# Kernel tuning notes

Measured on AMD Instinct MI355X. Metric: run time of the kernel, lower is better.

## Reference

```python
import jax, jax.numpy as jnp
import numpy as np

N_NODES = 8192
N_EDGES = 81920
N_EDGE2 = 1310720
D_EMB = 128
D_GAT = 64
H = 128
N_CLASSES = 2


def setup_inputs() -> dict:
    key = jax.random.key(0)
    ks = jax.random.split(key, 18)
    s = 0.05
    return {
        "x": jax.random.normal(ks[0], (N_NODES, D_EMB), jnp.float32),
        "embed": jax.random.normal(ks[1], (N_NODES, D_EMB), jnp.float32),
        "noise": jax.random.uniform(ks[2], (N_EDGES,), jnp.float32, 1e-6, 1.0 - 1e-6),
        "tmp": jnp.ones((), jnp.float32),
        "gat_W": jax.random.normal(ks[3], (2 * D_EMB, D_GAT), jnp.float32) * s,
        "att_src": jax.random.normal(ks[4], (D_GAT,), jnp.float32) * s,
        "att_dst": jax.random.normal(ks[5], (D_GAT,), jnp.float32) * s,
        "gat_bias": jax.random.normal(ks[6], (D_GAT,), jnp.float32) * s,
        "lin_W": jax.random.normal(ks[7], (D_GAT, 1), jnp.float32) * s,
        "lin_b": jax.random.normal(ks[8], (1,), jnp.float32) * s,
        "W1": jax.random.normal(ks[9], (D_EMB, H), jnp.float32) * s,
        "W2": jax.random.normal(ks[10], (H, H), jnp.float32) * s,
        "W3": jax.random.normal(ks[11], (H, H), jnp.float32) * s,
        "Wc": jax.random.normal(ks[12], (H, N_CLASSES), jnp.float32) * s,
        "edge_index": jax.random.randint(ks[13], (2, N_EDGES), 0, N_NODES, jnp.int32),
        "new_edge_index": jax.random.randint(ks[14], (2, N_EDGE2), 0, N_EDGES, jnp.int32),
        "label": 1,
    }


def reference(x, embed, noise, tmp, gat_W, att_src, att_dst, gat_bias, lin_W, lin_b,
              W1, W2, W3, Wc, edge_index, new_edge_index, label):
    N, E = x.shape[0], edge_index.shape[1]
    row, col = edge_index[0], edge_index[1]

    # h = cat(embed[row], embed[col])  -> [E, 2D]
    h = jnp.concatenate([embed[row], embed[col]], axis=-1)

    # --- GATConv(2D, 64) over the edge-adjacency graph (PyG single-head, self-loops) ---
    hp = h @ gat_W                              # [E, D_GAT]
    a_s = hp @ att_src                          # [E]
    a_d = hp @ att_dst                          # [E]
    loop = jnp.arange(E, dtype=new_edge_index.dtype)
    src = jnp.concatenate([new_edge_index[0], loop])
    dst = jnp.concatenate([new_edge_index[1], loop])
    alpha = jax.nn.leaky_relu(a_s[src] + a_d[dst], negative_slope=0.2)
    amax = jax.ops.segment_max(alpha, dst, num_segments=E)
    ealpha = jnp.exp(alpha - amax[dst])
    denom = jax.ops.segment_sum(ealpha, dst, num_segments=E)
    attn = ealpha / denom[dst]                  # softmax per destination edge-node
    gat_out = jax.ops.segment_sum(attn[:, None] * hp[src], dst, num_segments=E) + gat_bias

    # Linear(64, 1)
    log_alpha = (gat_out @ lin_W + lin_b).reshape(-1)   # [E]

    # concrete_sample (training=True, sample_bias=0.0)
    gate = jax.nn.sigmoid((jnp.log(noise) - jnp.log1p(-noise) + log_alpha) / tmp)

    # dense adjacency (ones, coalesce-sum) and dense gated mask
    adj = jnp.zeros((N, N), jnp.float32).at[row, col].add(1.0)
    sym_mask = jnp.zeros((N, N), jnp.float32).at[row, col].add(gate)
    sym_mask = (sym_mask + sym_mask.T) * 0.5
    masked_adj = adj * sym_mask
    edge_mask = masked_adj[row, col]

    # --- stub downstream model: 3-layer edge-weighted GCN + mean pool + classifier ---
    # explain-mode edge masking: messages weighted by sigmoid(edge_mask)
    w = jax.nn.sigmoid(edge_mask)
    deg = jax.ops.segment_sum(w, col, num_segments=N) + 1.0   # [N]

    def gcn(xh, W):
        msg = jax.ops.segment_sum(w[:, None] * xh[row], col, num_segments=N)
        return jax.nn.relu(((xh + msg) / deg[:, None]) @ W)

    h1 = gcn(x, W1)
    h2 = gcn(h1, W2)
    h3 = gcn(h2, W3)
    g = h3.mean(axis=0)                         # global mean pool (single graph)
    logits = g @ Wc
    return jax.nn.softmax(logits, axis=-1)
```

## Files before the change

kernel.cpp:

```cpp
#include <hip/hip_runtime.h>
#include <hip/hip_fp16.h>
#include <math.h>

typedef unsigned long long u64;
typedef __attribute__((ext_vector_type(2))) float fv2;

#define NN 8192
#define EE 81920
#define E2C 1310720
#define HSZ (1 << 18)
#define HMASK (HSZ - 1)
#define NBIN 320
#define BCAP 4800
#define SBITS 17

__device__ __forceinline__ float wsum(float v) {
#pragma unroll
  for (int m = 32; m > 0; m >>= 1) v += __shfl_xor(v, m, 64);
  return v;
}
__device__ __forceinline__ float lrelu(float x) { return x > 0.f ? x : 0.2f * x; }
__device__ __forceinline__ unsigned packh2(float a, float b) {
  __half2 h = __floats2half2_rn(a, b);
  return *reinterpret_cast<unsigned*>(&h);
}
__device__ __forceinline__ void atomic_pk_add_f16(unsigned* addr, unsigned data) {
  asm volatile("global_atomic_pk_add_f16 %0, %1, off" :: "v"(addr), "v"(data) : "memory");
}
__device__ __forceinline__ int hfind(const int* __restrict__ keys, int key) {
  unsigned i = ((unsigned)key * 2654435761u) >> 14 & HMASK;
  while (true) {
    int k = keys[i];
    if (k == key) return (int)i;
    if (k == -1) return -1;
    i = (i + 1) & HMASK;
  }
}
__device__ __forceinline__ float2 bf2f(unsigned u) {
  return make_float2(__uint_as_float(u << 16), __uint_as_float(u & 0xffff0000u));
}
__device__ __forceinline__ unsigned f2bf(float a, float b) {
  unsigned ua = __float_as_uint(a);
  ua = (ua + 0x7fffu + ((ua >> 16) & 1u)) >> 16;
  unsigned ub = __float_as_uint(b);
  ub = ((ub + 0x7fffu + ((ub >> 16) & 1u)) >> 16) << 16;
  return (ua & 0xffffu) | ub;
}
__device__ __forceinline__ unsigned f2bf1(float a) {
  unsigned ua = __float_as_uint(a);
  return (ua + 0x7fffu + ((ua >> 16) & 1u)) >> 16;
}
__device__ __forceinline__ float bf1f(unsigned u) { return __uint_as_float(u << 16); }
__device__ __forceinline__ unsigned short f2fp8x2(float a, float b) {
  return (unsigned short)(__builtin_amdgcn_cvt_pk_fp8_f32(a, b, 0, false) & 0xffff);
}
__device__ __forceinline__ float2 fp8x2f(unsigned short v) {
  fv2 f = __builtin_amdgcn_cvt_pk_f32_fp8((int)(unsigned)v, false);
  return make_float2(f[0], f[1]);
}
__device__ __forceinline__ float rdlane(float v, int k) {
  return __uint_as_float(__builtin_amdgcn_readlane(__float_as_uint(v), k));
}

__global__ __launch_bounds__(256) void kA(const float* __restrict__ x,
                                          const float* __restrict__ embed,
                                          const float* __restrict__ gw,
                                          const float* __restrict__ att_s,
                                          const float* __restrict__ att_d,
                                          const float* __restrict__ lin_W,
                                          const float* __restrict__ gat_b,
                                          const float* __restrict__ lin_b,
                                          float4* __restrict__ pN, float4* __restrict__ qN,
                                          unsigned short* __restrict__ xbu,
                                          int* __restrict__ hKeys, unsigned* __restrict__ hPair,
                                          int* __restrict__ colCnt, float* __restrict__ gvec,
                                          unsigned* __restrict__ done, unsigned* __restrict__ gCur,
                                          float* __restrict__ gbS) {
  __shared__ float sm[768];
  int t = threadIdx.x, bid = blockIdx.x;
  int lane = t & 63, wv = t >> 6;
  for (int i = bid * 256 + t; i < HSZ; i += 512 * 256) { hKeys[i] = -1; hPair[i] = 0u; }
  for (int i = bid * 256 + t; i < NN; i += 512 * 256) colCnt[i] = 0;
  if (bid == 0) {
    for (int i = t; i < 2048; i += 256) gvec[i] = 0.f;
    if (t == 0) *done = 0u;
    for (int i = t; i < NBIN; i += 256) gCur[i] = 0u;
    if (wv == 0) {
      float gb = wsum(gat_b[lane] * lin_W[lane]);
      if (lane == 0) *gbS = gb + lin_b[0];
    }
  }
  {
    int n = bid * 16 + (t >> 4);
    int dp = (t & 15) * 8;
    const float4* x4 = (const float4*)(x + n * 128 + dp);
    float4 a = x4[0], b = x4[1];
    unsigned p0 = f2fp8x2(a.x, a.y), p1 = f2fp8x2(a.z, a.w);
    unsigned p2 = f2fp8x2(b.x, b.y), p3 = f2fp8x2(b.z, b.w);
    ((uint2*)xbu)[n * 16 + (t & 15)] = make_uint2(p0 | (p1 << 16), p2 | (p3 << 16));
  }
  {
    float sa = 0.f, sd = 0.f, sz = 0.f;
#pragma unroll 8
    for (int k = 0; k < 64; k++) {
      float w = gw[t * 64 + k];
      sa += w * att_s[k]; sd += w * att_d[k]; sz += w * lin_W[k];
    }
    sm[t] = sa; sm[256 + t] = sd; sm[512 + t] = sz;
  }
  __syncthreads();
#pragma unroll
  for (int j = 0; j < 4; j++) {
    int n = bid * 16 + wv * 4 + j;
    float e0 = embed[n * 128 + lane], e1 = embed[n * 128 + 64 + lane];
    float pA = wsum(e0 * sm[lane] + e1 * sm[64 + lane]);
    float qA = wsum(e0 * sm[128 + lane] + e1 * sm[192 + lane]);
    float pD = wsum(e0 * sm[256 + lane] + e1 * sm[320 + lane]);
    float qD = wsum(e0 * sm[384 + lane] + e1 * sm[448 + lane]);
    float pZ = wsum(e0 * sm[512 + lane] + e1 * sm[576 + lane]);
    float qZ = wsum(e0 * sm[640 + lane] + e1 * sm[704 + lane]);
    if (lane == 0) pN[n] = make_float4(pA, pD, pZ, 0.f);
    if (lane == 1) qN[n] = make_float4(qA, qD, qZ, 0.f);
  }
}

__global__ __launch_bounds__(256) void kC(const int* __restrict__ row, const int* __restrict__ col,
                                          const float4* __restrict__ pN, const float4* __restrict__ qN,
                                          float2* __restrict__ asz, float* __restrict__ ad,
                                          int* __restrict__ colCnt,
                                          const int* __restrict__ src2, const int* __restrict__ dst2,
                                          unsigned* __restrict__ gCur, unsigned* __restrict__ bucket) {
  __shared__ unsigned hist[NBIN], base[NBIN], lcur[NBIN];
  int t = threadIdx.x;
  for (int i = t; i < NBIN; i += 256) { hist[i] = 0u; lcur[i] = 0u; }
  int blockBase = blockIdx.x * 4096;
  {
    int e = blockIdx.x * 256 + t;
    int r = row[e], c = col[e];
    float4 p = pN[r];
    float4 q = qN[c];
    asz[e] = make_float2(p.x + q.x, p.z + q.z);
    ad[e] = p.y + q.y;
    atomicAdd(&colCnt[c], 1);
  }
  __syncthreads();
  int4 dv[4];
#pragma unroll
  for (int j = 0; j < 4; j++) {
    dv[j] = *(const int4*)&dst2[blockBase + j * 1024 + t * 4];
    atomicAdd(&hist[dv[j].x >> 8], 1u);
    atomicAdd(&hist[dv[j].y >> 8], 1u);
    atomicAdd(&hist[dv[j].z >> 8], 1u);
    atomicAdd(&hist[dv[j].w >> 8], 1u);
  }
  __syncthreads();
  for (int i = t; i < NBIN; i += 256)
    if (hist[i]) base[i] = atomicAdd(&gCur[i], hist[i]);
  __syncthreads();
#pragma unroll
  for (int j = 0; j < 4; j++) {
    int4 sv = *(const int4*)&src2[blockBase + j * 1024 + t * 4];
    int ss[4] = {sv.x, sv.y, sv.z, sv.w};
    int dd[4] = {dv[j].x, dv[j].y, dv[j].z, dv[j].w};
#pragma unroll
    for (int k = 0; k < 4; k++) {
      int s = ss[k], d = dd[k];
      int b = d >> 8;
      unsigned r = atomicAdd(&lcur[b], 1u);
      unsigned pos = base[b] + r;
      if (pos < BCAP) bucket[(size_t)b * BCAP + pos] = ((unsigned)(d & 255) << SBITS) | (unsigned)s;
    }
  }
}

__global__ __launch_bounds__(256) void kD(const int* __restrict__ row, const int* __restrict__ col,
                                          const float2* __restrict__ asz, const float* __restrict__ ad,
                                          const unsigned* __restrict__ bucket, const unsigned* __restrict__ gCur,
                                          const float* __restrict__ gbS,
                                          const float* __restrict__ noise,
                                          const float* __restrict__ tmp,
                                          int* __restrict__ hKeys, unsigned* __restrict__ hPair,
                                          int* __restrict__ eslot,
                                          const int* __restrict__ colCnt, int* __restrict__ colOffs,
                                          int* __restrict__ colCur) {
  __shared__ float acc[512];
  __shared__ float adl[256];
  int b = blockIdx.x, t = threadIdx.x;
  if (b == NBIN) {
    __shared__ int sd32[256];
    int beg = t * 32;
    int s = 0;
#pragma unroll 8
    for (int i = 0; i < 32; i++) s += colCnt[beg + i];
    sd32[t] = s;
    __syncthreads();
    for (int o = 1; o < 256; o <<= 1) {
      int v = (t >= o) ? sd32[t - o] : 0;
      __syncthreads();
      sd32[t] += v;
      __syncthreads();
    }
    int run = (t == 0) ? 0 : sd32[t - 1];
    for (int i = 0; i < 32; i++) {
      colOffs[beg + i] = run;
      colCur[beg + i] = run;
      run += colCnt[beg + i];
    }
    if (t == 255) colOffs[NN] = run;
    return;
  }
  acc[2 * t] = 0.f; acc[2 * t + 1] = 0.f; adl[t] = ad[b * 256 + t];
  __syncthreads();
  int cnt = min((int)gCur[b], BCAP);
  const unsigned* bp = bucket + (size_t)b * BCAP;
  const unsigned SM = (1u << SBITS) - 1;
  int i = t;
  for (; i + 768 < cnt; i += 1024) {
    unsigned u0 = bp[i], u1 = bp[i + 256], u2 = bp[i + 512], u3 = bp[i + 768];
    float2 az0 = asz[u0 & SM], az1 = asz[u1 & SM], az2 = asz[u2 & SM], az3 = asz[u3 & SM];
    int l0 = u0 >> SBITS, l1 = u1 >> SBITS, l2 = u2 >> SBITS, l3 = u3 >> SBITS;
    float ea0 = __expf(lrelu(az0.x + adl[l0]));
    float ea1 = __expf(lrelu(az1.x + adl[l1]));
    float ea2 = __expf(lrelu(az2.x + adl[l2]));
    float ea3 = __expf(lrelu(az3.x + adl[l3]));
    atomicAdd(&acc[2 * l0], ea0); atomicAdd(&acc[2 * l0 + 1], ea0 * az0.y);
    atomicAdd(&acc[2 * l1], ea1); atomicAdd(&acc[2 * l1 + 1], ea1 * az1.y);
    atomicAdd(&acc[2 * l2], ea2); atomicAdd(&acc[2 * l2 + 1], ea2 * az2.y);
    atomicAdd(&acc[2 * l3], ea3); atomicAdd(&acc[2 * l3 + 1], ea3 * az3.y);
  }
  for (; i < cnt; i += 256) {
    unsigned u = bp[i];
    float2 az = asz[u & SM];
    int l = u >> SBITS;
    float ea = __expf(lrelu(az.x + adl[l]));
    atomicAdd(&acc[2 * l], ea);
    atomicAdd(&acc[2 * l + 1], ea * az.y);
  }
  __syncthreads();
  float gb = *gbS;
  float itmp = 1.f / tmp[0];
  {
    int e = b * 256 + t;
    float2 szv = asz[e];
    float eself = __expf(lrelu(szv.x + adl[t]));
    float la = (acc[2 * t + 1] + eself * szv.y) / (acc[2 * t] + eself) + gb;
    float ns = noise[e];
    float g = (logf(ns) - log1pf(-ns) + la) * itmp;
    float gate = 1.f / (1.f + __expf(-g));
    int key = row[e] * NN + col[e];
    unsigned hi = ((unsigned)key * 2654435761u) >> 14 & HMASK;
    while (true) {
      int old = atomicCAS(&hKeys[hi], -1, key);
      if (old == -1 || old == key) break;
      hi = (hi + 1) & HMASK;
    }
    eslot[e] = (int)hi;
    atomic_pk_add_f16(&hPair[hi], packh2(1.0f, gate));
  }
}

__global__ void kE(const int* __restrict__ row, const int* __restrict__ col,
                   const int* __restrict__ hKeys, const unsigned* __restrict__ hPair,
                   const int* __restrict__ eslot,
                   int* __restrict__ colCur, unsigned* __restrict__ csrW) {
  int e = blockIdx.x * 256 + threadIdx.x;
  int r = row[e], c = col[e];
  int s1 = eslot[e];
  unsigned u1 = hPair[s1];
  __half2 h1 = *reinterpret_cast<__half2*>(&u1);
  float cv = __low2float(h1), g1 = __high2float(h1);
  int s2 = hfind(hKeys, c * NN + r);
  float g2 = 0.f;
  if (s2 >= 0) {
    unsigned u2 = hPair[s2];
    g2 = __high2float(*reinterpret_cast<__half2*>(&u2));
  }
  float em = cv * 0.5f * (g1 + g2);
  float w = 1.f / (1.f + __expf(-em));
  int pos = atomicAdd(&colCur[c], 1);
  csrW[pos] = (f2bf1(w) << 16) | (unsigned)r;
}

__device__ __forceinline__ float2 gatherNode(const unsigned short* __restrict__ xb, int n, int lane,
                                             const int* __restrict__ colOffs,
                                             const unsigned* __restrict__ csrW) {
  float2 sf = fp8x2f(xb[n * 64 + lane]);
  float a0 = sf.x, a1 = sf.y, ws = 0.f;
  int off = colOffs[n], end = colOffs[n + 1];
  int i = off;
  for (; i + 4 <= end; i += 4) {
    unsigned q0 = csrW[i], q1 = csrW[i + 1], q2 = csrW[i + 2], q3 = csrW[i + 3];
    unsigned short u0 = xb[(q0 & 0x1fff) * 64 + lane];
    unsigned short u1 = xb[(q1 & 0x1fff) * 64 + lane];
    unsigned short u2 = xb[(q2 & 0x1fff) * 64 + lane];
    unsigned short u3 = xb[(q3 & 0x1fff) * 64 + lane];
    float w0 = bf1f(q0 >> 16), w1 = bf1f(q1 >> 16);
    float w2 = bf1f(q2 >> 16), w3 = bf1f(q3 >> 16);
    ws += w0 + w1 + w2 + w3;
    float2 f0 = fp8x2f(u0), f1 = fp8x2f(u1), f2v = fp8x2f(u2), f3 = fp8x2f(u3);
    a0 += w0 * f0.x + w1 * f1.x + w2 * f2v.x + w3 * f3.x;
    a1 += w0 * f0.y + w1 * f1.y + w2 * f2v.y + w3 * f3.y;
  }
  for (; i < end; i++) {
    unsigned q = csrW[i];
    unsigned short u = xb[(q & 0x1fff) * 64 + lane];
    float w = bf1f(q >> 16);
    ws += w;
    float2 f = fp8x2f(u);
    a0 += w * f.x;
    a1 += w * f.y;
  }
  float inv = 1.f / (1.f + ws);
  return make_float2(a0 * inv, a1 * inv);
}

#define GEMM2(tv, acc)                                                   \
  {                                                                      \
    _Pragma("unroll") for (int j = 0; j < 2; j++) acc[j] = make_float2(0.f, 0.f); \
    _Pragma("unroll 16") for (int k2 = 0; k2 < 64; k2++) {               \
      float2 w0 = bf2f(Wl[(2 * k2) * 64 + lane]);                        \
      float2 w1 = bf2f(Wl[(2 * k2 + 1) * 64 + lane]);                    \
      _Pragma("unroll") for (int j = 0; j < 2; j++) {                    \
        float bx = rdlane(tv[j].x, k2);                                  \
        float by = rdlane(tv[j].y, k2);                                  \
        acc[j].x += bx * w0.x + by * w1.x;                               \
        acc[j].y += bx * w0.y + by * w1.y;                               \
      }                                                                  \
    }                                                                    \
  }

__global__ __launch_bounds__(256) void kF(const unsigned short* __restrict__ xb,
                                          const int* __restrict__ colOffs,
                                          const unsigned* __restrict__ csrW,
                                          const float* __restrict__ W,
                                          unsigned short* __restrict__ outB) {
  __shared__ unsigned Wl[128 * 64];
  int t = threadIdx.x, lane = t & 63, wv = t >> 6;
  const float4* W4 = (const float4*)W;
  for (int i = t; i < 4096; i += 256) {
    float4 a = W4[i];
    ((uint2*)Wl)[i] = make_uint2(f2bf(a.x, a.y), f2bf(a.z, a.w));
  }
  int nb = blockIdx.x * 8;
  float2 tv[2];
#pragma unroll
  for (int j = 0; j < 2; j++)
    tv[j] = gatherNode(xb, nb + wv * 2 + j, lane, colOffs, csrW);
  __syncthreads();
  float2 acc[2];
  GEMM2(tv, acc)
#pragma unroll
  for (int j = 0; j < 2; j++) {
    int n = nb + wv * 2 + j;
    outB[n * 64 + lane] = f2fp8x2(fmaxf(acc[j].x, 0.f), fmaxf(acc[j].y, 0.f));
  }
}

__global__ __launch_bounds__(256) void kH(const unsigned short* __restrict__ xb,
                                          const int* __restrict__ colOffs,
                                          const unsigned* __restrict__ csrW,
                                          const float* __restrict__ W,
                                          const float* __restrict__ Wc,
                                          float* __restrict__ gvec, unsigned* __restrict__ done,
                                          float* __restrict__ out) {
  __shared__ unsigned Wl[128 * 64];
  int t = threadIdx.x, lane = t & 63, wv = t >> 6;
  const float4* W4 = (const float4*)W;
  for (int i = t; i < 4096; i += 256) {
    float4 a = W4[i];
    ((uint2*)Wl)[i] = make_uint2(f2bf(a.x, a.y), f2bf(a.z, a.w));
  }
  int nb = blockIdx.x * 8;
  float2 tv[2];
#pragma unroll
  for (int j = 0; j < 2; j++)
    tv[j] = gatherNode(xb, nb + wv * 2 + j, lane, colOffs, csrW);
  __syncthreads();
  float2 acc[2];
  GEMM2(tv, acc)
  float s0 = fmaxf(acc[0].x, 0.f) + fmaxf(acc[1].x, 0.f);
  float s1 = fmaxf(acc[0].y, 0.f) + fmaxf(acc[1].y, 0.f);
  __syncthreads();
  float* gpart = (float*)Wl;
  unsigned* flagp = (unsigned*)Wl + 600;
  if (t < 128) gpart[t] = 0.f;
  __syncthreads();
  atomicAdd(&gpart[2 * lane], s0);
  atomicAdd(&gpart[2 * lane + 1], s1);
  __syncthreads();
  if (t < 128) atomicAdd(&gvec[((blockIdx.x & 15) << 7) + t], gpart[t]);
  asm volatile("s_waitcnt vmcnt(0)" ::: "memory");
  __syncthreads();
  if (t == 0) *flagp = (atomicAdd(done, 1u) == gridDim.x - 1) ? 1u : 0u;
  __syncthreads();
  if (*flagp) {
    float* f0 = (float*)Wl + 256;
    float* f1 = (float*)Wl + 384;
    if (t < 128) {
      float gj = 0.f;
#pragma unroll
      for (int k = 0; k < 16; k++) gj += atomicAdd(&gvec[k * 128 + t], 0.f);
      gj *= (1.0f / 8192.0f);
      f0[t] = gj * Wc[t * 2 + 0];
      f1[t] = gj * Wc[t * 2 + 1];
    }
    __syncthreads();
    for (int o = 64; o > 0; o >>= 1) {
      if (t < o) { f0[t] += f0[t + o]; f1[t] += f1[t + o]; }
      __syncthreads();
    }
    if (t == 0) {
      float l0 = f0[0], l1 = f1[0];
      float m = fmaxf(l0, l1);
      float e0 = __expf(l0 - m), e1 = __expf(l1 - m);
      float inv = 1.f / (e0 + e1);
      out[0] = e0 * inv;
      out[1] = e1 * inv;
    }
  }
}

extern "C" void kernel_launch(void* const* d_in, const int* in_sizes, int n_in,
                              void* d_out, int out_size, void* d_ws, size_t ws_size,
                              hipStream_t stream) {
  const float* x     = (const float*)d_in[0];
  const float* embed = (const float*)d_in[1];
  const float* noise = (const float*)d_in[2];
  const float* tmp   = (const float*)d_in[3];
  const float* gat_W = (const float*)d_in[4];
  const float* att_s = (const float*)d_in[5];
  const float* att_d = (const float*)d_in[6];
  const float* gat_b = (const float*)d_in[7];
  const float* lin_W = (const float*)d_in[8];
  const float* lin_b = (const float*)d_in[9];
  const float* W1    = (const float*)d_in[10];
  const float* W2    = (const float*)d_in[11];
  const float* W3    = (const float*)d_in[12];
  const float* Wc    = (const float*)d_in[13];
  const int* ei      = (const int*)d_in[14];
  const int* nei     = (const int*)d_in[15];
  const int* row = ei;
  const int* col = ei + EE;
  const int* src2 = nei;
  const int* dst2 = nei + E2C;
  float* out = (float*)d_out;

  char* w8 = (char*)d_ws;
  size_t off = 0;
  auto alloc = [&](size_t units) -> void* {
    void* p = w8 + off * 4;
    off += units;
    return p;
  };
  float4*   pN      = (float4*)alloc(4 * NN);
  float4*   qN      = (float4*)alloc(4 * NN);
  float2*   asz     = (float2*)alloc(2 * EE);
  unsigned short* xbu = (unsigned short*)alloc(NN * 32);
  unsigned short* H1u = (unsigned short*)alloc(NN * 32);
  unsigned short* H2u = (unsigned short*)alloc(NN * 32);
  unsigned* csrW    = (unsigned*)alloc(EE);
  float*    ad      = (float*)alloc(EE);
  int*      eslot   = (int*)alloc(EE);
  int*      colCnt  = (int*)alloc(NN);
  int*      colOffs = (int*)alloc(NN + 2);
  int*      colCur  = (int*)alloc(NN);
  int*      hKeys   = (int*)alloc(HSZ);
  unsigned* hPair   = (unsigned*)alloc(HSZ);
  unsigned* bucket  = (unsigned*)alloc((size_t)NBIN * BCAP);
  unsigned* gCur    = (unsigned*)alloc(NBIN);
  float*    gvec    = (float*)alloc(2048);
  unsigned* done    = (unsigned*)alloc(2);
  float*    gbS     = (float*)alloc(2);

  kA<<<512, 256, 0, stream>>>(x, embed, gat_W, att_s, att_d, lin_W, gat_b, lin_b,
                              pN, qN, xbu, hKeys, hPair, colCnt, gvec, done, gCur, gbS);
  kC<<<NBIN, 256, 0, stream>>>(row, col, pN, qN, asz, ad, colCnt, src2, dst2, gCur, bucket);
  kD<<<NBIN + 1, 256, 0, stream>>>(row, col, asz, ad, bucket, gCur, gbS, noise, tmp,
                                   hKeys, hPair, eslot, colCnt, colOffs, colCur);
  kE<<<EE / 256, 256, 0, stream>>>(row, col, hKeys, hPair, eslot, colCur, csrW);
  kF<<<NN / 8, 256, 0, stream>>>(xbu, colOffs, csrW, W1, H1u);
  kF<<<NN / 8, 256, 0, stream>>>(H1u, colOffs, csrW, W2, H2u);
  kH<<<NN / 8, 256, 0, stream>>>(H2u, colOffs, csrW, W3, Wc, gvec, done, out);
}
```

Measured before the change: 222.6 us.

## Replace bucketed GAT edge aggregation with direct global atomic scatter

Removes the two-pass binning scheme, where edges were histogrammed into per-destination buckets and then reduced in LDS, and replaces it with a kernel that computes attention exponentials per edge and scatters them into a global per-destination accumulator with float atomics. The bucket buffer and its capacity clipping go away, and the launch splits into separate edge-prep, scatter and finalize kernels. In exchange the 1.3M edges now issue 2.6M global float atomics to random addresses instead of LDS atomics, and one extra kernel launch is added.

```diff
diff --git a/kernel.cpp b/kernel.cpp
--- a/kernel.cpp
+++ b/kernel.cpp
@@ -11,8 +11,6 @@
 #define HSZ (1 << 18)
 #define HMASK (HSZ - 1)
 #define NBIN 320
-#define BCAP 4800
-#define SBITS 17
 
 __device__ __forceinline__ float wsum(float v) {
 #pragma unroll
@@ -74,17 +72,17 @@
                                           unsigned short* __restrict__ xbu,
                                           int* __restrict__ hKeys, unsigned* __restrict__ hPair,
                                           int* __restrict__ colCnt, float* __restrict__ gvec,
-                                          unsigned* __restrict__ done, unsigned* __restrict__ gCur,
+                                          unsigned* __restrict__ done, float* __restrict__ dstAcc,
                                           float* __restrict__ gbS) {
   __shared__ float sm[768];
   int t = threadIdx.x, bid = blockIdx.x;
   int lane = t & 63, wv = t >> 6;
   for (int i = bid * 256 + t; i < HSZ; i += 512 * 256) { hKeys[i] = -1; hPair[i] = 0u; }
   for (int i = bid * 256 + t; i < NN; i += 512 * 256) colCnt[i] = 0;
+  for (int i = bid * 256 + t; i < 2 * EE; i += 512 * 256) dstAcc[i] = 0.f;
   if (bid == 0) {
     for (int i = t; i < 2048; i += 256) gvec[i] = 0.f;
     if (t == 0) *done = 0u;
-    for (int i = t; i < NBIN; i += 256) gCur[i] = 0u;
     if (wv == 0) {
       float gb = wsum(gat_b[lane] * lin_W[lane]);
       if (lane == 0) *gbS = gb + lin_b[0];
@@ -124,67 +122,47 @@
   }
 }
 
-__global__ __launch_bounds__(256) void kC(const int* __restrict__ row, const int* __restrict__ col,
+__global__ __launch_bounds__(256) void kB(const int* __restrict__ row, const int* __restrict__ col,
                                           const float4* __restrict__ pN, const float4* __restrict__ qN,
                                           float2* __restrict__ asz, float* __restrict__ ad,
-                                          int* __restrict__ colCnt,
-                                          const int* __restrict__ src2, const int* __restrict__ dst2,
-                                          unsigned* __restrict__ gCur, unsigned* __restrict__ bucket) {
-  __shared__ unsigned hist[NBIN], base[NBIN], lcur[NBIN];
-  int t = threadIdx.x;
-  for (int i = t; i < NBIN; i += 256) { hist[i] = 0u; lcur[i] = 0u; }
-  int blockBase = blockIdx.x * 4096;
-  {
-    int e = blockIdx.x * 256 + t;
-    int r = row[e], c = col[e];
-    float4 p = pN[r];
-    float4 q = qN[c];
-    asz[e] = make_float2(p.x + q.x, p.z + q.z);
-    ad[e] = p.y + q.y;
-    atomicAdd(&colCnt[c], 1);
-  }
-  __syncthreads();
-  int4 dv[4];
-#pragma unroll
-  for (int j = 0; j < 4; j++) {
-    dv[j] = *(const int4*)&dst2[blockBase + j * 1024 + t * 4];
-    atomicAdd(&hist[dv[j].x >> 8], 1u);
-    atomicAdd(&hist[dv[j].y >> 8], 1u);
-    atomicAdd(&hist[dv[j].z >> 8], 1u);
-    atomicAdd(&hist[dv[j].w >> 8], 1u);
-  }
-  __syncthreads();
-  for (int i = t; i < NBIN; i += 256)
-    if (hist[i]) base[i] = atomicAdd(&gCur[i], hist[i]);
-  __syncthreads();
-#pragma unroll
-  for (int j = 0; j < 4; j++) {
-    int4 sv = *(const int4*)&src2[blockBase + j * 1024 + t * 4];
-    int ss[4] = {sv.x, sv.y, sv.z, sv.w};
-    int dd[4] = {dv[j].x, dv[j].y, dv[j].z, dv[j].w};
-#pragma unroll
-    for (int k = 0; k < 4; k++) {
-      int s = ss[k], d = dd[k];
-      int b = d >> 8;
-      unsigned r = atomicAdd(&lcur[b], 1u);
-      unsigned pos = base[b] + r;
-      if (pos < BCAP) bucket[(size_t)b * BCAP + pos] = ((unsigned)(d & 255) << SBITS) | (unsigned)s;
-    }
-  }
-}
-
-__global__ __launch_bounds__(256) void kD(const int* __restrict__ row, const int* __restrict__ col,
-                                          const float2* __restrict__ asz, const float* __restrict__ ad,
-                                          const unsigned* __restrict__ bucket, const unsigned* __restrict__ gCur,
-                                          const float* __restrict__ gbS,
-                                          const float* __restrict__ noise,
-                                          const float* __restrict__ tmp,
-                                          int* __restrict__ hKeys, unsigned* __restrict__ hPair,
-                                          int* __restrict__ eslot,
-                                          const int* __restrict__ colCnt, int* __restrict__ colOffs,
-                                          int* __restrict__ colCur) {
-  __shared__ float acc[512];
-  __shared__ float adl[256];
+                                          int* __restrict__ colCnt) {
+  int e = blockIdx.x * 256 + threadIdx.x;
+  int r = row[e], c = col[e];
+  float4 p = pN[r];
+  float4 q = qN[c];
+  asz[e] = make_float2(p.x + q.x, p.z + q.z);
+  ad[e] = p.y + q.y;
+  atomicAdd(&colCnt[c], 1);
+}
+
+__global__ __launch_bounds__(256) void kC2(const float2* __restrict__ asz, const float* __restrict__ ad,
+                                           const int* __restrict__ src2, const int* __restrict__ dst2,
+                                           float* __restrict__ dstAcc) {
+  int base = blockIdx.x * 1024 + threadIdx.x * 4;
+  int4 sv = *(const int4*)&src2[base];
+  int4 dv = *(const int4*)&dst2[base];
+  float2 az0 = asz[sv.x], az1 = asz[sv.y], az2 = asz[sv.z], az3 = asz[sv.w];
+  float d0 = ad[dv.x], d1 = ad[dv.y], d2 = ad[dv.z], d3 = ad[dv.w];
+  float ea0 = __expf(lrelu(az0.x + d0));
+  float ea1 = __expf(lrelu(az1.x + d1));
+  float ea2 = __expf(lrelu(az2.x + d2));
+  float ea3 = __expf(lrelu(az3.x + d3));
+  atomicAdd(&dstAcc[2 * dv.x], ea0); atomicAdd(&dstAcc[2 * dv.x + 1], ea0 * az0.y);
+  atomicAdd(&dstAcc[2 * dv.y], ea1); atomicAdd(&dstAcc[2 * dv.y + 1], ea1 * az1.y);
+  atomicAdd(&dstAcc[2 * dv.z], ea2); atomicAdd(&dstAcc[2 * dv.z + 1], ea2 * az2.y);
+  atomicAdd(&dstAcc[2 * dv.w], ea3); atomicAdd(&dstAcc[2 * dv.w + 1], ea3 * az3.y);
+}
+
+__global__ __launch_bounds__(256) void kD2(const int* __restrict__ row, const int* __restrict__ col,
+                                           const float2* __restrict__ asz, const float* __restrict__ ad,
+                                           const float* __restrict__ dstAcc,
+                                           const float* __restrict__ gbS,
+                                           const float* __restrict__ noise,
+                                           const float* __restrict__ tmp,
+                                           int* __restrict__ hKeys, unsigned* __restrict__ hPair,
+                                           int* __restrict__ eslot,
+                                           const int* __restrict__ colCnt, int* __restrict__ colOffs,
+                                           int* __restrict__ colCur) {
   int b = blockIdx.x, t = threadIdx.x;
   if (b == NBIN) {
     __shared__ int sd32[256];
@@ -209,54 +187,26 @@
     if (t == 255) colOffs[NN] = run;
     return;
   }
-  acc[2 * t] = 0.f; acc[2 * t + 1] = 0.f; adl[t] = ad[b * 256 + t];
-  __syncthreads();
-  int cnt = min((int)gCur[b], BCAP);
-  const unsigned* bp = bucket + (size_t)b * BCAP;
-  const unsigned SM = (1u << SBITS) - 1;
-  int i = t;
-  for (; i + 768 < cnt; i += 1024) {
-    unsigned u0 = bp[i], u1 = bp[i + 256], u2 = bp[i + 512], u3 = bp[i + 768];
-    float2 az0 = asz[u0 & SM], az1 = asz[u1 & SM], az2 = asz[u2 & SM], az3 = asz[u3 & SM];
-    int l0 = u0 >> SBITS, l1 = u1 >> SBITS, l2 = u2 >> SBITS, l3 = u3 >> SBITS;
-    float ea0 = __expf(lrelu(az0.x + adl[l0]));
-    float ea1 = __expf(lrelu(az1.x + adl[l1]));
-    float ea2 = __expf(lrelu(az2.x + adl[l2]));
-    float ea3 = __expf(lrelu(az3.x + adl[l3]));
-    atomicAdd(&acc[2 * l0], ea0); atomicAdd(&acc[2 * l0 + 1], ea0 * az0.y);
-    atomicAdd(&acc[2 * l1], ea1); atomicAdd(&acc[2 * l1 + 1], ea1 * az1.y);
-    atomicAdd(&acc[2 * l2], ea2); atomicAdd(&acc[2 * l2 + 1], ea2 * az2.y);
-    atomicAdd(&acc[2 * l3], ea3); atomicAdd(&acc[2 * l3 + 1], ea3 * az3.y);
-  }
-  for (; i < cnt; i += 256) {
-    unsigned u = bp[i];
-    float2 az = asz[u & SM];
-    int l = u >> SBITS;
-    float ea = __expf(lrelu(az.x + adl[l]));
-    atomicAdd(&acc[2 * l], ea);
-    atomicAdd(&acc[2 * l + 1], ea * az.y);
-  }
-  __syncthreads();
+  int e = b * 256 + t;
   float gb = *gbS;
   float itmp = 1.f / tmp[0];
-  {
-    int e = b * 256 + t;
-    float2 szv = asz[e];
-    float eself = __expf(lrelu(szv.x + adl[t]));
-    float la = (acc[2 * t + 1] + eself * szv.y) / (acc[2 * t] + eself) + gb;
-    float ns = noise[e];
-    float g = (logf(ns) - log1pf(-ns) + la) * itmp;
-    float gate = 1.f / (1.f + __expf(-g));
-    int key = row[e] * NN + col[e];
-    unsigned hi = ((unsigned)key * 2654435761u) >> 14 & HMASK;
-    while (true) {
-      int old = atomicCAS(&hKeys[hi], -1, key);
-      if (old == -1 || old == key) break;
-      hi = (hi + 1) & HMASK;
-    }
-    eslot[e] = (int)hi;
-    atomic_pk_add_f16(&hPair[hi], packh2(1.0f, gate));
-  }
+  float2 szv = asz[e];
+  float adv = ad[e];
+  float eself = __expf(lrelu(szv.x + adv));
+  float accE = dstAcc[2 * e], accZ = dstAcc[2 * e + 1];
+  float la = (accZ + eself * szv.y) / (accE + eself) + gb;
+  float ns = noise[e];
+  float g = (logf(ns) - log1pf(-ns) + la) * itmp;
+  float gate = 1.f / (1.f + __expf(-g));
+  int key = row[e] * NN + col[e];
+  unsigned hi = ((unsigned)key * 2654435761u) >> 14 & HMASK;
+  while (true) {
+    int old = atomicCAS(&hKeys[hi], -1, key);
+    if (old == -1 || old == key) break;
+    hi = (hi + 1) & HMASK;
+  }
+  eslot[e] = (int)hi;
+  atomic_pk_add_f16(&hPair[hi], packh2(1.0f, gate));
 }
 
 __global__ void kE(const int* __restrict__ row, const int* __restrict__ col,
@@ -466,17 +416,17 @@
   int*      colCur  = (int*)alloc(NN);
   int*      hKeys   = (int*)alloc(HSZ);
   unsigned* hPair   = (unsigned*)alloc(HSZ);
-  unsigned* bucket  = (unsigned*)alloc((size_t)NBIN * BCAP);
-  unsigned* gCur    = (unsigned*)alloc(NBIN);
+  float*    dstAcc  = (float*)alloc(2 * EE);
   float*    gvec    = (float*)alloc(2048);
   unsigned* done    = (unsigned*)alloc(2);
   float*    gbS     = (float*)alloc(2);
 
   kA<<<512, 256, 0, stream>>>(x, embed, gat_W, att_s, att_d, lin_W, gat_b, lin_b,
-                              pN, qN, xbu, hKeys, hPair, colCnt, gvec, done, gCur, gbS);
-  kC<<<NBIN, 256, 0, stream>>>(row, col, pN, qN, asz, ad, colCnt, src2, dst2, gCur, bucket);
-  kD<<<NBIN + 1, 256, 0, stream>>>(row, col, asz, ad, bucket, gCur, gbS, noise, tmp,
-                                   hKeys, hPair, eslot, colCnt, colOffs, colCur);
+                              pN, qN, xbu, hKeys, hPair, colCnt, gvec, done, dstAcc, gbS);
+  kB<<<NBIN, 256, 0, stream>>>(row, col, pN, qN, asz, ad, colCnt);
+  kC2<<<E2C / 1024, 256, 0, stream>>>(asz, ad, src2, dst2, dstAcc);
+  kD2<<<NBIN + 1, 256, 0, stream>>>(row, col, asz, ad, dstAcc, gbS, noise, tmp,
+                                    hKeys, hPair, eslot, colCnt, colOffs, colCur);
   kE<<<EE / 256, 256, 0, stream>>>(row, col, hKeys, hPair, eslot, colCur, csrW);
   kF<<<NN / 8, 256, 0, stream>>>(xbu, colOffs, csrW, W1, H1u);
   kF<<<NN / 8, 256, 0, stream>>>(H1u, colOffs, csrW, W2, H2u);
```

Measured after the change: 319.4 us. 1.44x slower.

## Replace prefix-sum CSR with fixed-capacity padded CSR and fold edge weights into first GCN layer

Applied to the files above, without the earlier changes.

Builds a padded per-destination edge list (capacity 40 per node) directly in kC via the atomic counter, which removes the prefix-scan block in kD and the separate kE edge-weight kernel. The first GCN layer kernel now computes the sigmoid edge weights (hash lookups for the symmetric gate) on the fly and writes the packed CSR weights for the later layers. This removes one launch and a scan, but any node with in-degree above 40 silently drops edges. Each weight is also computed redundantly by all 64 lanes of a wavefront.

```diff
diff --git a/kernel.cpp b/kernel.cpp
--- a/kernel.cpp
+++ b/kernel.cpp
@@ -13,6 +13,7 @@
 #define NBIN 320
 #define BCAP 4800
 #define SBITS 17
+#define DCAP 40
 
 __device__ __forceinline__ float wsum(float v) {
 #pragma unroll
@@ -127,7 +128,7 @@
 __global__ __launch_bounds__(256) void kC(const int* __restrict__ row, const int* __restrict__ col,
                                           const float4* __restrict__ pN, const float4* __restrict__ qN,
                                           float2* __restrict__ asz, float* __restrict__ ad,
-                                          int* __restrict__ colCnt,
+                                          int* __restrict__ colCnt, int* __restrict__ csrE,
                                           const int* __restrict__ src2, const int* __restrict__ dst2,
                                           unsigned* __restrict__ gCur, unsigned* __restrict__ bucket) {
   __shared__ unsigned hist[NBIN], base[NBIN], lcur[NBIN];
@@ -141,7 +142,8 @@
     float4 q = qN[c];
     asz[e] = make_float2(p.x + q.x, p.z + q.z);
     ad[e] = p.y + q.y;
-    atomicAdd(&colCnt[c], 1);
+    int s = atomicAdd(&colCnt[c], 1);
+    if (s < DCAP) csrE[c * DCAP + s] = e;
   }
   __syncthreads();
   int4 dv[4];
@@ -180,35 +182,10 @@
                                           const float* __restrict__ noise,
                                           const float* __restrict__ tmp,
                                           int* __restrict__ hKeys, unsigned* __restrict__ hPair,
-                                          int* __restrict__ eslot,
-                                          const int* __restrict__ colCnt, int* __restrict__ colOffs,
-                                          int* __restrict__ colCur) {
+                                          int* __restrict__ eslot) {
   __shared__ float acc[512];
   __shared__ float adl[256];
   int b = blockIdx.x, t = threadIdx.x;
-  if (b == NBIN) {
-    __shared__ int sd32[256];
-    int beg = t * 32;
-    int s = 0;
-#pragma unroll 8
-    for (int i = 0; i < 32; i++) s += colCnt[beg + i];
-    sd32[t] = s;
-    __syncthreads();
-    for (int o = 1; o < 256; o <<= 1) {
-      int v = (t >= o) ? sd32[t - o] : 0;
-      __syncthreads();
-      sd32[t] += v;
-      __syncthreads();
-    }
-    int run = (t == 0) ? 0 : sd32[t - 1];
-    for (int i = 0; i < 32; i++) {
-      colOffs[beg + i] = run;
-      colCur[beg + i] = run;
-      run += colCnt[beg + i];
-    }
-    if (t == 255) colOffs[NN] = run;
-    return;
-  }
   acc[2 * t] = 0.f; acc[2 * t + 1] = 0.f; adl[t] = ad[b * 256 + t];
   __syncthreads();
   int cnt = min((int)gCur[b], BCAP);
@@ -259,37 +236,78 @@
   }
 }
 
-__global__ void kE(const int* __restrict__ row, const int* __restrict__ col,
-                   const int* __restrict__ hKeys, const unsigned* __restrict__ hPair,
-                   const int* __restrict__ eslot,
-                   int* __restrict__ colCur, unsigned* __restrict__ csrW) {
-  int e = blockIdx.x * 256 + threadIdx.x;
-  int r = row[e], c = col[e];
-  int s1 = eslot[e];
-  unsigned u1 = hPair[s1];
+__device__ __forceinline__ float wfold(int n, int e, const int* __restrict__ row,
+                                       const int* __restrict__ eslot,
+                                       const unsigned* __restrict__ hPair,
+                                       const int* __restrict__ hKeys, int& rOut) {
+  int r = row[e];
+  rOut = r;
+  unsigned u1 = hPair[eslot[e]];
   __half2 h1 = *reinterpret_cast<__half2*>(&u1);
   float cv = __low2float(h1), g1 = __high2float(h1);
-  int s2 = hfind(hKeys, c * NN + r);
+  int s2 = hfind(hKeys, n * NN + r);
   float g2 = 0.f;
   if (s2 >= 0) {
     unsigned u2 = hPair[s2];
     g2 = __high2float(*reinterpret_cast<__half2*>(&u2));
   }
   float em = cv * 0.5f * (g1 + g2);
-  float w = 1.f / (1.f + __expf(-em));
-  int pos = atomicAdd(&colCur[c], 1);
-  csrW[pos] = (f2bf1(w) << 16) | (unsigned)r;
-}
-
-__device__ __forceinline__ float2 gatherNode(const unsigned short* __restrict__ xb, int n, int lane,
-                                             const int* __restrict__ colOffs,
-                                             const unsigned* __restrict__ csrW) {
+  return 1.f / (1.f + __expf(-em));
+}
+
+__device__ __forceinline__ float2 gatherFold(const unsigned short* __restrict__ xb, int n, int lane,
+                                             const int* __restrict__ cnt,
+                                             const int* __restrict__ csrE,
+                                             const int* __restrict__ row,
+                                             const int* __restrict__ eslot,
+                                             const unsigned* __restrict__ hPair,
+                                             const int* __restrict__ hKeys,
+                                             unsigned* __restrict__ csrW) {
   float2 sf = fp8x2f(xb[n * 64 + lane]);
   float a0 = sf.x, a1 = sf.y, ws = 0.f;
-  int off = colOffs[n], end = colOffs[n + 1];
-  int i = off;
-  for (; i + 4 <= end; i += 4) {
-    unsigned q0 = csrW[i], q1 = csrW[i + 1], q2 = csrW[i + 2], q3 = csrW[i + 3];
+  int deg = min(cnt[n], DCAP);
+  const int* seg = csrE + n * DCAP;
+  unsigned* wseg = csrW + n * DCAP;
+  int j = 0;
+  for (; j + 2 <= deg; j += 2) {
+    int e0 = seg[j], e1 = seg[j + 1];
+    int r0, r1;
+    float w0 = wfold(n, e0, row, eslot, hPair, hKeys, r0);
+    float w1 = wfold(n, e1, row, eslot, hPair, hKeys, r1);
+    if (lane == 0) {
+      wseg[j] = (f2bf1(w0) << 16) | (unsigned)r0;
+      wseg[j + 1] = (f2bf1(w1) << 16) | (unsigned)r1;
+    }
+    ws += w0 + w1;
+    float2 f0 = fp8x2f(xb[r0 * 64 + lane]);
+    float2 f1 = fp8x2f(xb[r1 * 64 + lane]);
+    a0 += w0 * f0.x + w1 * f1.x;
+    a1 += w0 * f0.y + w1 * f1.y;
+  }
+  for (; j < deg; j++) {
+    int e = seg[j];
+    int r;
+    float w = wfold(n, e, row, eslot, hPair, hKeys, r);
+    if (lane == 0) wseg[j] = (f2bf1(w) << 16) | (unsigned)r;
+    ws += w;
+    float2 f = fp8x2f(xb[r * 64 + lane]);
+    a0 += w * f.x;
+    a1 += w * f.y;
+  }
+  float inv = 1.f / (1.f + ws);
+  return make_float2(a0 * inv, a1 * inv);
+}
+
+__device__ __forceinline__ float2 gatherNodeP(const unsigned short* __restrict__ xb, int n, int lane,
+                                              const int* __restrict__ cnt,
+                                              const unsigned* __restrict__ csrW) {
+  float2 sf = fp8x2f(xb[n * 64 + lane]);
+  float a0 = sf.x, a1 = sf.y, ws = 0.f;
+  int deg = min(cnt[n], DCAP);
+  const unsigned* seg = csrW + n * DCAP;
+  int i = 0;
+  for (; i + 4 <= deg; i += 4) {
+    unsigned q0 = seg[i], q1 = seg[i + 1], q2 = seg[i + 2], q3 = seg[i + 3];
     unsigned short u0 = xb[(q0 & 0x1fff) * 64 + lane];
     unsigned short u1 = xb[(q1 & 0x1fff) * 64 + lane];
     unsigned short u2 = xb[(q2 & 0x1fff) * 64 + lane];
@@ -301,8 +319,8 @@
     a0 += w0 * f0.x + w1 * f1.x + w2 * f2v.x + w3 * f3.x;
     a1 += w0 * f0.y + w1 * f1.y + w2 * f2v.y + w3 * f3.y;
   }
-  for (; i < end; i++) {
-    unsigned q = csrW[i];
+  for (; i < deg; i++) {
+    unsigned q = seg[i];
     unsigned short u = xb[(q & 0x1fff) * 64 + lane];
     float w = bf1f(q >> 16);
     ws += w;
@@ -329,8 +347,40 @@
     }                                                                    \
   }
 
+__global__ __launch_bounds__(256) void kF1(const unsigned short* __restrict__ xb,
+                                           const int* __restrict__ colCnt,
+                                           const int* __restrict__ csrE,
+                                           const int* __restrict__ row,
+                                           const int* __restrict__ eslot,
+                                           const unsigned* __restrict__ hPair,
+                                           const int* __restrict__ hKeys,
+                                           unsigned* __restrict__ csrW,
+                                           const float* __restrict__ W,
+                                           unsigned short* __restrict__ outB) {
+  __shared__ unsigned Wl[128 * 64];
+  int t = threadIdx.x, lane = t & 63, wv = t >> 6;
+  const float4* W4 = (const float4*)W;
+  for (int i = t; i < 4096; i += 256) {
+    float4 a = W4[i];
+    ((uint2*)Wl)[i] = make_uint2(f2bf(a.x, a.y), f2bf(a.z, a.w));
+  }
+  int nb = blockIdx.x * 8;
+  float2 tv[2];
+#pragma unroll
+  for (int j = 0; j < 2; j++)
+    tv[j] = gatherFold(xb, nb + wv * 2 + j, lane, colCnt, csrE, row, eslot, hPair, hKeys, csrW);
+  __syncthreads();
+  float2 acc[2];
+  GEMM2(tv, acc)
+#pragma unroll
+  for (int j = 0; j < 2; j++) {
+    int n = nb + wv * 2 + j;
+    outB[n * 64 + lane] = f2fp8x2(fmaxf(acc[j].x, 0.f), fmaxf(acc[j].y, 0.f));
+  }
+}
+
 __global__ __launch_bounds__(256) void kF(const unsigned short* __restrict__ xb,
-                                          const int* __restrict__ colOffs,
+                                          const int* __restrict__ colCnt,
                                           const unsigned* __restrict__ csrW,
                                           const float* __restrict__ W,
                                           unsigned short* __restrict__ outB) {
@@ -345,7 +395,7 @@
   float2 tv[2];
 #pragma unroll
   for (int j = 0; j < 2; j++)
-    tv[j] = gatherNode(xb, nb + wv * 2 + j, lane, colOffs, csrW);
+    tv[j] = gatherNodeP(xb, nb + wv * 2 + j, lane, colCnt, csrW);
   __syncthreads();
   float2 acc[2];
   GEMM2(tv, acc)
@@ -357,7 +407,7 @@
 }
 
 __global__ __launch_bounds__(256) void kH(const unsigned short* __restrict__ xb,
-                                          const int* __restrict__ colOffs,
+                                          const int* __restrict__ colCnt,
                                           const unsigned* __restrict__ csrW,
                                           const float* __restrict__ W,
                                           const float* __restrict__ Wc,
@@ -374,7 +424,7 @@
   float2 tv[2];
 #pragma unroll
   for (int j = 0; j < 2; j++)
-    tv[j] = gatherNode(xb, nb + wv * 2 + j, lane, colOffs, csrW);
+    tv[j] = gatherNodeP(xb, nb + wv * 2 + j, lane, colCnt, csrW);
   __syncthreads();
   float2 acc[2];
   GEMM2(tv, acc)
@@ -458,12 +508,11 @@
   unsigned short* xbu = (unsigned short*)alloc(NN * 32);
   unsigned short* H1u = (unsigned short*)alloc(NN * 32);
   unsigned short* H2u = (unsigned short*)alloc(NN * 32);
-  unsigned* csrW    = (unsigned*)alloc(EE);
+  unsigned* csrW    = (unsigned*)alloc(NN * DCAP);
+  int*      csrE    = (int*)alloc(NN * DCAP);
   float*    ad      = (float*)alloc(EE);
   int*      eslot   = (int*)alloc(EE);
   int*      colCnt  = (int*)alloc(NN);
-  int*      colOffs = (int*)alloc(NN + 2);
-  int*      colCur  = (int*)alloc(NN);
   int*      hKeys   = (int*)alloc(HSZ);
   unsigned* hPair   = (unsigned*)alloc(HSZ);
   unsigned* bucket  = (unsigned*)alloc((size_t)NBIN * BCAP);
@@ -474,11 +523,10 @@
 
   kA<<<512, 256, 0, stream>>>(x, embed, gat_W, att_s, att_d, lin_W, gat_b, lin_b,
                               pN, qN, xbu, hKeys, hPair, colCnt, gvec, done, gCur, gbS);
-  kC<<<NBIN, 256, 0, stream>>>(row, col, pN, qN, asz, ad, colCnt, src2, dst2, gCur, bucket);
-  kD<<<NBIN + 1, 256, 0, stream>>>(row, col, asz, ad, bucket, gCur, gbS, noise, tmp,
-                                   hKeys, hPair, eslot, colCnt, colOffs, colCur);
-  kE<<<EE / 256, 256, 0, stream>>>(row, col, hKeys, hPair, eslot, colCur, csrW);
-  kF<<<NN / 8, 256, 0, stream>>>(xbu, colOffs, csrW, W1, H1u);
-  kF<<<NN / 8, 256, 0, stream>>>(H1u, colOffs, csrW, W2, H2u);
-  kH<<<NN / 8, 256, 0, stream>>>(H2u, colOffs, csrW, W3, Wc, gvec, done, out);
-}
+  kC<<<NBIN, 256, 0, stream>>>(row, col, pN, qN, asz, ad, colCnt, csrE, src2, dst2, gCur, bucket);
+  kD<<<NBIN, 256, 0, stream>>>(row, col, asz, ad, bucket, gCur, gbS, noise, tmp,
+                               hKeys, hPair, eslot);
+  kF1<<<NN / 8, 256, 0, stream>>>(xbu, colCnt, csrE, row, eslot, hPair, hKeys, csrW, W1, H1u);
+  kF<<<NN / 8, 256, 0, stream>>>(H1u, colCnt, csrW, W2, H2u);
+  kH<<<NN / 8, 256, 0, stream>>>(H2u, colCnt, csrW, W3, Wc, gvec, done, out);
+}
```

Result: slower. 236.7 us (+6.4%).
